# Performance work log

Measured on AMD Instinct MI355X. Metric: run time of the kernel, lower is better.

## Reference

```python
import jax, jax.numpy as jnp
import numpy as np

B, T, C, H = 8, 2048, 1024, 1024
SCALE = 1.0 / np.sqrt(H).astype(np.float32)


def setup_inputs() -> dict:
    key = jax.random.key(0)
    kx, kq, kk, kv = jax.random.split(key, 4)
    x = jax.random.normal(kx, (B, T, C), dtype=jnp.float32)
    # Linear(C -> H, bias=False): store weights as [C, H] so y = x @ W
    Wq = jax.random.normal(kq, (C, H), dtype=jnp.float32) * (1.0 / np.sqrt(C))
    Wk = jax.random.normal(kk, (C, H), dtype=jnp.float32) * (1.0 / np.sqrt(C))
    Wv = jax.random.normal(kv, (C, H), dtype=jnp.float32) * (1.0 / np.sqrt(C))
    return {"x": x, "Wq": Wq, "Wk": Wk, "Wv": Wv}


def reference(x, Wq, Wk, Wv):
    # Projections
    Q = jnp.einsum('btc,ch->bth', x, Wq)
    K = jnp.einsum('btc,ch->bth', x, Wk)
    V = jnp.einsum('btc,ch->bth', x, Wv)
    t = x.shape[1]
    # Scaled dot-product scores with causal mask
    attn = jnp.einsum('bqh,bkh->bqk', Q, K) * SCALE  # [B,T,T]
    causal = jnp.tril(jnp.ones((t, t), dtype=bool))
    attn = jnp.where(causal, attn, -jnp.inf)
    scores = jax.nn.softmax(attn, axis=-1)
    # dropout p=0.0 (eval/deterministic) -> identity
    out = jnp.einsum('bqk,bkh->bqh', scores, V)
    return out
```

## Files before the change

kernel.cpp:

```cpp
#include <hip/hip_runtime.h>


#define BM 128
#define BN 128
#define BK 32

typedef __attribute__((ext_vector_type(8))) __bf16 bf16x8;
typedef __attribute__((ext_vector_type(4))) float floatx4;

__device__ __forceinline__ unsigned short f2bf(float f) {
  unsigned int u = __float_as_uint(f);
  u += 0x7fffu + ((u >> 16) & 1u);
  return (unsigned short)(u >> 16);
}
__device__ __forceinline__ float bf2f(unsigned short s) {
  return __uint_as_float(((unsigned int)s) << 16);
}

__device__ __forceinline__ void gload_lds16(const unsigned short* g, unsigned short* l) {
  __builtin_amdgcn_global_load_lds(
      (const __attribute__((address_space(1))) void*)g,
      (__attribute__((address_space(3))) void*)l,
      16, 0, 0);
}


__device__ __forceinline__ void gemm_mainloop(
    const unsigned short* __restrict__ A, int lda,
    const unsigned short* __restrict__ Bt, int ldb,
    int m0, int n0, int kTiles,
    unsigned short* As, unsigned short* Bs,
    floatx4 (&acc)[4][4])
{
  const int tid  = threadIdx.x;
  const int wave = tid >> 6;
  const int lane = tid & 63;
  const int wr = wave >> 1;
  const int wc = wave & 1;

  const int c0 = wave * 2;
  const int c1 = c0 + 1;
  const int r0 = c0 * 16 + (lane >> 2);
  const int r1 = c1 * 16 + (lane >> 2);
  const int ck = (lane & 3) * 8;

  const unsigned short* pA0 = A  + (size_t)(m0 + r0) * lda + ck;
  const unsigned short* pA1 = A  + (size_t)(m0 + r1) * lda + ck;
  const unsigned short* pB0 = Bt + (size_t)(n0 + r0) * ldb + ck;
  const unsigned short* pB1 = Bt + (size_t)(n0 + r1) * ldb + ck;

  unsigned short* lA0 = As + c0 * 512;
  unsigned short* lA1 = As + c1 * 512;
  unsigned short* lB0 = Bs + c0 * 512;
  unsigned short* lB1 = Bs + c1 * 512;

  const int fr = lane & 15;
  const int kq = (lane >> 4) * 8;

  for (int kt = 0; kt < kTiles; ++kt) {
    __syncthreads();
    gload_lds16(pA0, lA0);
    gload_lds16(pA1, lA1);
    gload_lds16(pB0, lB0);
    gload_lds16(pB1, lB1);
    pA0 += BK; pA1 += BK; pB0 += BK; pB1 += BK;
    __syncthreads();

    bf16x8 af[4], bg[4];
#pragma unroll
    for (int i = 0; i < 4; ++i)
      af[i] = *(const bf16x8*)(As + ((wr * 64 + i * 16 + fr) * BK + kq));
#pragma unroll
    for (int j = 0; j < 4; ++j)
      bg[j] = *(const bf16x8*)(Bs + ((wc * 64 + j * 16 + fr) * BK + kq));
#pragma unroll
    for (int i = 0; i < 4; ++i)
#pragma unroll
      for (int j = 0; j < 4; ++j)
        acc[i][j] = __builtin_amdgcn_mfma_f32_16x16x32_bf16(af[i], bg[j], acc[i][j], 0, 0, 0);
  }
}

#define ACC_INIT(acc)                         \
  do {                                        \
    floatx4 z_ = {0.f, 0.f, 0.f, 0.f};        \
    _Pragma("unroll")                         \
    for (int i_ = 0; i_ < 4; ++i_)            \
      _Pragma("unroll")                       \
      for (int j_ = 0; j_ < 4; ++j_)          \
        acc[i_][j_] = z_;                     \
  } while (0)


__global__ void cvt_x_kernel(const float* __restrict__ x, unsigned short* __restrict__ xb) {
  int idx = (blockIdx.x * 256 + threadIdx.x) * 4;
  float4 v = *(const float4*)(x + idx);
  ushort4 o;
  o.x = f2bf(v.x); o.y = f2bf(v.y); o.z = f2bf(v.z); o.w = f2bf(v.w);
  *(ushort4*)(xb + idx) = o;
}

__global__ void cvt_w_kernel(const float* __restrict__ W, unsigned short* __restrict__ Wt) {
  __shared__ unsigned short tile[64][65];
  const int k0 = blockIdx.x * 64, n0 = blockIdx.y * 64;
  const int tid = threadIdx.x, tx = tid & 63, ty = tid >> 6;
#pragma unroll
  for (int r = 0; r < 64; r += 4)
    tile[r + ty][tx] = f2bf(W[(size_t)(k0 + r + ty) * 1024 + (n0 + tx)]);
  __syncthreads();
#pragma unroll
  for (int r = 0; r < 64; r += 4)
    Wt[(size_t)(n0 + r + ty) * 1024 + (k0 + tx)] = tile[tx][r + ty];
}

__global__ void zero_l_kernel(float* __restrict__ l) {
  l[blockIdx.x * 256 + threadIdx.x] = 0.f;
}

__global__ __launch_bounds__(512, 2) void gemm_qkv_kernel(
    const unsigned short* __restrict__ xb,
    const unsigned short* __restrict__ Wt,
    unsigned short* __restrict__ Q,
    unsigned short* __restrict__ K,
    unsigned short* __restrict__ V)
{
  __shared__ __align__(16) unsigned short lds[49152];

  const int bid = blockIdx.x;
  const int xcd = bid & 7;
  const int local = bid >> 3;
  const int mi = xcd * 8 + (local & 7);
  const int ni = local >> 3;
  const int m0 = mi * 256;
  const int n0 = ni * 256;

  const int tid = threadIdx.x;
  const int w = tid >> 6;
  const int l = tid & 63;
  const int wr = w >> 2;
  const int wc = w & 3;

  const int sr0 = w * 16 + (l >> 2);
  const int scs = (((l & 3) ^ ((l >> 3) & 3)) << 3);

  const unsigned short* pA0 = xb + (size_t)(m0 + sr0) * 1024 + scs;
  const unsigned short* pA1 = xb + (size_t)(m0 + 128 + sr0) * 1024 + scs;
  const unsigned short* pB0 = Wt + (size_t)(n0 + sr0) * 1024 + scs;
  const unsigned short* pB1 = Wt + (size_t)(n0 + 128 + sr0) * 1024 + scs;

  const int stgW = w * 512;

#define STAGE4(slot)                                             \
  do {                                                           \
    unsigned short* _sA = &lds[(slot) * 8192 + stgW];            \
    unsigned short* _sB = &lds[24576 + (slot) * 8192 + stgW];    \
    gload_lds16(pA0, _sA);                                       \
    gload_lds16(pA1, _sA + 4096);                                \
    gload_lds16(pB0, _sB);                                       \
    gload_lds16(pB1, _sB + 4096);                                \
    pA0 += 32; pA1 += 32; pB0 += 32; pB1 += 32;                  \
  } while (0)

  const int fr = l & 15;
  const int q  = l >> 4;
  const int cks = ((q ^ ((fr >> 1) & 3)) << 3);
  const int aOff = (wr * 128 + fr) * 32 + cks;
  const int bOff = (wc * 64 + fr) * 32 + cks;

  floatx4 acc[8][4];
  {
    floatx4 z = {0.f, 0.f, 0.f, 0.f};
#pragma unroll
    for (int i = 0; i < 8; ++i)
#pragma unroll
      for (int j = 0; j < 4; ++j)
        acc[i][j] = z;
  }

  STAGE4(0);
  STAGE4(1);
  asm volatile("s_waitcnt vmcnt(4)" ::: "memory");
  __builtin_amdgcn_s_barrier();

  bf16x8 a[8], b0[4], b1[4];
  {
    const unsigned short* sA = &lds[0];
    const unsigned short* sB = &lds[24576];
#pragma unroll
    for (int j = 0; j < 4; ++j) b0[j] = *(const bf16x8*)(sB + bOff + j * 512);
    a[0] = *(const bf16x8*)(sA + aOff);
    a[1] = *(const bf16x8*)(sA + aOff + 512);
  }

#define MFMA_PAIR(I0, BU)                                                           \
  do {                                                                              \
    __builtin_amdgcn_s_setprio(1);                                                  \
    _Pragma("unroll")                                                               \
    for (int j = 0; j < 4; ++j) {                                                   \
      acc[(I0)][j] =                                                                \
          __builtin_amdgcn_mfma_f32_16x16x32_bf16(a[(I0)], BU[j], acc[(I0)][j], 0, 0, 0); \
      acc[(I0) + 1][j] =                                                            \
          __builtin_amdgcn_mfma_f32_16x16x32_bf16(a[(I0) + 1], BU[j], acc[(I0) + 1][j], 0, 0, 0); \
    }                                                                               \
    __builtin_amdgcn_s_setprio(0);                                                  \
  } while (0)

#define ITER(KT, BU, BP)                                                  \
  do {                                                                    \
    const int nslot = (slot == 2) ? 0 : slot + 1;                         \
    const int sslot = (nslot == 2) ? 0 : nslot + 1;                       \
    const unsigned short* sA  = &lds[slot * 8192];                        \
    const unsigned short* sAn = &lds[nslot * 8192];                       \
    const unsigned short* sBn = &lds[24576 + nslot * 8192];               \
    unsigned short* dA = &lds[sslot * 8192 + stgW];                       \
    unsigned short* dB = &lds[24576 + sslot * 8192 + stgW];               \
    const bool doStage = ((KT) < 30);                                     \
    const bool doNext  = ((KT) < 31);                                     \
     \
    a[2] = *(const bf16x8*)(sA + aOff + 2 * 512);                         \
    a[3] = *(const bf16x8*)(sA + aOff + 3 * 512);                         \
    if (doStage) gload_lds16(pA0, dA);                                    \
    __builtin_amdgcn_s_barrier();                                         \
    MFMA_PAIR(0, BU);                                                     \
    __builtin_amdgcn_s_barrier();                                         \
                \
    a[4] = *(const bf16x8*)(sA + aOff + 4 * 512);                         \
    a[5] = *(const bf16x8*)(sA + aOff + 5 * 512);                         \
    if (doStage) gload_lds16(pA1, dA + 4096);                             \
    __builtin_amdgcn_s_barrier();                                         \
    MFMA_PAIR(2, BU);                                                     \
    __builtin_amdgcn_s_barrier();                                         \
                \
    a[6] = *(const bf16x8*)(sA + aOff + 6 * 512);                         \
    a[7] = *(const bf16x8*)(sA + aOff + 7 * 512);                         \
    if (doStage) gload_lds16(pB0, dB);                                    \
    __builtin_amdgcn_s_barrier();                                         \
    MFMA_PAIR(4, BU);                                                     \
    __builtin_amdgcn_s_barrier();                                         \
    \
    if (doNext) {                                                         \
      if (doStage) asm volatile("s_waitcnt vmcnt(3)" ::: "memory");       \
      else         asm volatile("s_waitcnt vmcnt(0)" ::: "memory");       \
      __builtin_amdgcn_s_barrier();                                       \
      _Pragma("unroll")                                                   \
      for (int j = 0; j < 4; ++j)                                         \
        BP[j] = *(const bf16x8*)(sBn + bOff + j * 512);                   \
      a[0] = *(const bf16x8*)(sAn + aOff);                                \
      a[1] = *(const bf16x8*)(sAn + aOff + 512);                          \
    }                                                                     \
    if (doStage) {                                                        \
      gload_lds16(pB1, dB + 4096);                                       \
      pA0 += 32; pA1 += 32; pB0 += 32; pB1 += 32;                         \
    }                                                                     \
    MFMA_PAIR(6, BU);                                                     \
    __builtin_amdgcn_s_barrier();                                         \
    slot = nslot;                                                         \
  } while (0)

  int slot = 0;
#pragma unroll 1
  for (int kt2 = 0; kt2 < 16; ++kt2) {
    const int kt = kt2 * 2;
    ITER(kt, b0, b1);
    ITER(kt + 1, b1, b0);
  }
#undef ITER
#undef MFMA_PAIR
#undef STAGE4

  unsigned short* const dsts[3] = {Q, K, V};
  unsigned short* D = dsts[n0 >> 10];
  const int ncol0 = n0 & 1023;

  const int rb = m0 + wr * 128 + (q << 2);
  const int cb = ncol0 + wc * 64 + fr;
#pragma unroll
  for (int i = 0; i < 8; ++i)
#pragma unroll
    for (int j = 0; j < 4; ++j)
#pragma unroll
      for (int r = 0; r < 4; ++r)
        D[(size_t)(rb + i * 16 + r) * 1024 + (cb + j * 16)] = f2bf(acc[i][j][r]);
}

__global__ void transpose_v_kernel(const unsigned short* __restrict__ V,
                                   unsigned short* __restrict__ Vt) {
  __shared__ unsigned short tile[64][68];
  const int b = blockIdx.z;
  const int t0 = blockIdx.x * 64, h0 = blockIdx.y * 64;
  const int tid = threadIdx.x;
  const int cx = (tid & 15) * 4;
  const int ry = tid >> 4;
  const unsigned short* Vb = V + (size_t)b * 2048 * 1024;
#pragma unroll
  for (int r = 0; r < 64; r += 16) {
    ushort4 v = *(const ushort4*)(Vb + (size_t)(t0 + r + ry) * 1024 + (h0 + cx));
    *(ushort4*)&tile[r + ry][cx] = v;
  }
  __syncthreads();
  unsigned short* Vtb = Vt + (size_t)b * 1024 * 2048;
#pragma unroll
  for (int r = 0; r < 64; r += 16) {
    const int h = r + ry;
    ushort4 o;
    o.x = tile[cx][h]; o.y = tile[cx + 1][h]; o.z = tile[cx + 2][h]; o.w = tile[cx + 3][h];
    *(ushort4*)(Vtb + (size_t)(h0 + h) * 2048 + (t0 + cx)) = o;
  }
}

__global__ __launch_bounds__(256) void gemm_scores_kernel(
    const unsigned short* __restrict__ Q,
    const unsigned short* __restrict__ K,
    unsigned short* __restrict__ S,
    float* __restrict__ lsum)
{
  const int b = blockIdx.x & 7;
  const int t = blockIdx.x >> 3;
  int mi = (int)((sqrtf(8.f * (float)t + 1.f) - 1.f) * 0.5f);
  while ((mi + 1) * (mi + 2) / 2 <= t) ++mi;
  while (mi * (mi + 1) / 2 > t) --mi;
  const int ni = t - mi * (mi + 1) / 2;
  const int m0 = mi * BM;
  const int n0 = ni * BN;

  __shared__ __align__(16) unsigned short As[BM * BK];
  __shared__ __align__(16) unsigned short Bs[BN * BK];
  floatx4 acc[4][4];
  ACC_INIT(acc);
  const unsigned short* Qb = Q + (size_t)b * 2048 * 1024;
  const unsigned short* Kb = K + (size_t)b * 2048 * 1024;
  gemm_mainloop(Qb, 1024, Kb, 1024, m0, n0, 1024 / BK, As, Bs, acc);

  unsigned short* Sb = S + (size_t)b * 2048 * 2048;
  float* lb = lsum + b * 2048;
  const int tid = threadIdx.x, wave = tid >> 6, lane = tid & 63;
  const int wr = wave >> 1, wc = wave & 1;
  const int rb = m0 + wr * 64 + ((lane >> 4) << 2);
  const int cb = n0 + wc * 64 + (lane & 15);

  float rsum[4][4];
#pragma unroll
  for (int i = 0; i < 4; ++i)
#pragma unroll
    for (int r = 0; r < 4; ++r)
      rsum[i][r] = 0.f;

#pragma unroll
  for (int i = 0; i < 4; ++i)
#pragma unroll
    for (int j = 0; j < 4; ++j)
#pragma unroll
      for (int r = 0; r < 4; ++r) {
        const int tq = rb + i * 16 + r;
        const int tk = cb + j * 16;
        float e = 0.f;
        if (tk <= tq) e = __expf(acc[i][j][r] * 0.03125f);
        const unsigned short h = f2bf(e);
        Sb[(size_t)tq * 2048 + tk] = h;
        rsum[i][r] += bf2f(h);
      }

#pragma unroll
  for (int off = 1; off < 16; off <<= 1)
#pragma unroll
    for (int i = 0; i < 4; ++i)
#pragma unroll
      for (int r = 0; r < 4; ++r)
        rsum[i][r] += __shfl_xor(rsum[i][r], off, 64);

  if ((lane & 15) == 0) {
#pragma unroll
    for (int i = 0; i < 4; ++i)
#pragma unroll
      for (int r = 0; r < 4; ++r)
        atomicAdd(&lb[rb + i * 16 + r], rsum[i][r]);
  }
}

__global__ __launch_bounds__(256) void gemm_pv_kernel(
    const unsigned short* __restrict__ S,
    const unsigned short* __restrict__ Vt,
    const float* __restrict__ lsum,
    float* __restrict__ out)
{
  const int b = blockIdx.x & 7;
  const int r2 = blockIdx.x >> 3;
  const int mi = 15 - (r2 >> 3);
  const int ni = r2 & 7;
  const int m0 = mi * BM;
  const int n0 = ni * BN;

  __shared__ __align__(16) unsigned short As[BM * BK];
  __shared__ __align__(16) unsigned short Bs[BN * BK];
  floatx4 acc[4][4];
  ACC_INIT(acc);
  const unsigned short* Pb = S  + (size_t)b * 2048 * 2048;
  const unsigned short* Vb = Vt + (size_t)b * 1024 * 2048;
  const int kTiles = m0 / BK + BM / BK;
  gemm_mainloop(Pb, 2048, Vb, 2048, m0, n0, kTiles, As, Bs, acc);

  float* Ob = out + (size_t)b * 2048 * 1024;
  const float* lb = lsum + b * 2048;
  const int tid = threadIdx.x, wave = tid >> 6, lane = tid & 63;
  const int wr = wave >> 1, wc = wave & 1;
  const int rb = m0 + wr * 64 + ((lane >> 4) << 2);
  const int cb = n0 + wc * 64 + (lane & 15);

  float inv[4][4];
#pragma unroll
  for (int i = 0; i < 4; ++i)
#pragma unroll
    for (int r = 0; r < 4; ++r)
      inv[i][r] = 1.0f / lb[rb + i * 16 + r];

#pragma unroll
  for (int i = 0; i < 4; ++i)
#pragma unroll
    for (int j = 0; j < 4; ++j)
#pragma unroll
      for (int r = 0; r < 4; ++r)
        Ob[(size_t)(rb + i * 16 + r) * 1024 + (cb + j * 16)] = acc[i][j][r] * inv[i][r];
}


extern "C" void kernel_launch(void* const* d_in, const int* in_sizes, int n_in,
                              void* d_out, int out_size, void* d_ws, size_t ws_size,
                              hipStream_t stream) {
  const float* x  = (const float*)d_in[0];
  const float* Wq = (const float*)d_in[1];
  const float* Wk = (const float*)d_in[2];
  const float* Wv = (const float*)d_in[3];
  float* out = (float*)d_out;

  char* ws = (char*)d_ws;
  unsigned short* xb  = (unsigned short*)(ws);
  unsigned short* Wt  = (unsigned short*)(ws + 33554432ull);
  unsigned short* Q   = (unsigned short*)(ws + 39845888ull);
  unsigned short* K   = (unsigned short*)(ws + 73400320ull);
  unsigned short* V   = (unsigned short*)(ws + 106954752ull);
  unsigned short* Vt  = (unsigned short*)(ws + 140509184ull);
  unsigned short* S   = (unsigned short*)(ws + 174063616ull);
  float*          l   = (float*)ws;

  cvt_x_kernel<<<16384, 256, 0, stream>>>(x, xb);
  dim3 gw(16, 16);
  cvt_w_kernel<<<gw, 256, 0, stream>>>(Wq, Wt);
  cvt_w_kernel<<<gw, 256, 0, stream>>>(Wk, Wt + 1024 * 1024);
  cvt_w_kernel<<<gw, 256, 0, stream>>>(Wv, Wt + 2 * 1024 * 1024);

  gemm_qkv_kernel<<<768, 512, 0, stream>>>(xb, Wt, Q, K, V);

  transpose_v_kernel<<<dim3(32, 16, 8), 256, 0, stream>>>(V, Vt);
  zero_l_kernel<<<64, 256, 0, stream>>>(l);
  gemm_scores_kernel<<<8 * 136, 256, 0, stream>>>(Q, K, S, l);
  gemm_pv_kernel<<<1024, 256, 0, stream>>>(S, Vt, l, out);
}
```

Baseline: 378.7 us.

## Widen attention GEMM K-tile to 64 with XOR-swizzled LDS and fuse prep kernels

The shared mainloop used by the scores and PV GEMMs now stages 64-wide K tiles instead of 32, using an XOR-swizzled LDS layout to avoid bank conflicts. This halves the number of barrier pairs per K step. The three conversion kernels and the zeroing kernel are merged into a single prep launch, and the row-sum buffer moves to its own workspace region instead of aliasing xb. The QKV macro's final staging load is moved into a helper macro and issued before the wait instead of after it, which changes the vmcnt accounting.

```diff
diff --git a/kernel.cpp b/kernel.cpp
--- a/kernel.cpp
+++ b/kernel.cpp
@@ -1,9 +1,5 @@
 #include <hip/hip_runtime.h>
 
-
-#define BM 128
-#define BN 128
-#define BK 32
 
 typedef __attribute__((ext_vector_type(8))) __bf16 bf16x8;
 typedef __attribute__((ext_vector_type(4))) float floatx4;
@@ -24,11 +20,10 @@
       16, 0, 0);
 }
 
-
-__device__ __forceinline__ void gemm_mainloop(
+__device__ __forceinline__ void gemm_mainloop64(
     const unsigned short* __restrict__ A, int lda,
     const unsigned short* __restrict__ Bt, int ldb,
-    int m0, int n0, int kTiles,
+    int m0, int n0, int kSteps,
     unsigned short* As, unsigned short* Bs,
     floatx4 (&acc)[4][4])
 {
@@ -38,41 +33,48 @@
   const int wr = wave >> 1;
   const int wc = wave & 1;
 
-  const int c0 = wave * 2;
-  const int c1 = c0 + 1;
-  const int r0 = c0 * 16 + (lane >> 2);
-  const int r1 = c1 * 16 + (lane >> 2);
-  const int ck = (lane & 3) * 8;
-
-  const unsigned short* pA0 = A  + (size_t)(m0 + r0) * lda + ck;
-  const unsigned short* pA1 = A  + (size_t)(m0 + r1) * lda + ck;
-  const unsigned short* pB0 = Bt + (size_t)(n0 + r0) * ldb + ck;
-  const unsigned short* pB1 = Bt + (size_t)(n0 + r1) * ldb + ck;
-
-  unsigned short* lA0 = As + c0 * 512;
-  unsigned short* lA1 = As + c1 * 512;
-  unsigned short* lB0 = Bs + c0 * 512;
-  unsigned short* lB1 = Bs + c1 * 512;
+  const int rowIn = lane >> 3;
+  const int srcChunk = (((lane & 7) ^ rowIn) << 3);
+
+  const unsigned short* gA = A  + (size_t)(m0 + wave * 32 + rowIn) * lda + srcChunk;
+  const unsigned short* gB = Bt + (size_t)(n0 + wave * 32 + rowIn) * ldb + srcChunk;
+  const int lda8 = lda << 3;
+  const int ldb8 = ldb << 3;
 
   const int fr = lane & 15;
-  const int kq = (lane >> 4) * 8;
-
-  for (int kt = 0; kt < kTiles; ++kt) {
+  const int kq = lane >> 4;
+  const int ac0 = ((kq ^ (fr & 7)) << 3);
+  const int ac1 = (((4 + kq) ^ (fr & 7)) << 3);
+
+  for (int kt = 0; kt < kSteps; ++kt) {
     __syncthreads();
-    gload_lds16(pA0, lA0);
-    gload_lds16(pA1, lA1);
-    gload_lds16(pB0, lB0);
-    gload_lds16(pB1, lB1);
-    pA0 += BK; pA1 += BK; pB0 += BK; pB1 += BK;
+#pragma unroll
+    for (int i = 0; i < 4; ++i)
+      gload_lds16(gA + i * lda8, As + (wave * 32 + i * 8) * 64);
+#pragma unroll
+    for (int i = 0; i < 4; ++i)
+      gload_lds16(gB + i * ldb8, Bs + (wave * 32 + i * 8) * 64);
+    gA += 64; gB += 64;
     __syncthreads();
 
     bf16x8 af[4], bg[4];
 #pragma unroll
     for (int i = 0; i < 4; ++i)
-      af[i] = *(const bf16x8*)(As + ((wr * 64 + i * 16 + fr) * BK + kq));
+      af[i] = *(const bf16x8*)(As + (wr * 64 + i * 16 + fr) * 64 + ac0);
 #pragma unroll
     for (int j = 0; j < 4; ++j)
-      bg[j] = *(const bf16x8*)(Bs + ((wc * 64 + j * 16 + fr) * BK + kq));
+      bg[j] = *(const bf16x8*)(Bs + (wc * 64 + j * 16 + fr) * 64 + ac0);
+#pragma unroll
+    for (int i = 0; i < 4; ++i)
+#pragma unroll
+      for (int j = 0; j < 4; ++j)
+        acc[i][j] = __builtin_amdgcn_mfma_f32_16x16x32_bf16(af[i], bg[j], acc[i][j], 0, 0, 0);
+#pragma unroll
+    for (int i = 0; i < 4; ++i)
+      af[i] = *(const bf16x8*)(As + (wr * 64 + i * 16 + fr) * 64 + ac1);
+#pragma unroll
+    for (int j = 0; j < 4; ++j)
+      bg[j] = *(const bf16x8*)(Bs + (wc * 64 + j * 16 + fr) * 64 + ac1);
 #pragma unroll
     for (int i = 0; i < 4; ++i)
 #pragma unroll
@@ -92,29 +94,41 @@
   } while (0)
 
 
-__global__ void cvt_x_kernel(const float* __restrict__ x, unsigned short* __restrict__ xb) {
-  int idx = (blockIdx.x * 256 + threadIdx.x) * 4;
-  float4 v = *(const float4*)(x + idx);
-  ushort4 o;
-  o.x = f2bf(v.x); o.y = f2bf(v.y); o.z = f2bf(v.z); o.w = f2bf(v.w);
-  *(ushort4*)(xb + idx) = o;
-}
-
-__global__ void cvt_w_kernel(const float* __restrict__ W, unsigned short* __restrict__ Wt) {
-  __shared__ unsigned short tile[64][65];
-  const int k0 = blockIdx.x * 64, n0 = blockIdx.y * 64;
-  const int tid = threadIdx.x, tx = tid & 63, ty = tid >> 6;
-#pragma unroll
-  for (int r = 0; r < 64; r += 4)
-    tile[r + ty][tx] = f2bf(W[(size_t)(k0 + r + ty) * 1024 + (n0 + tx)]);
-  __syncthreads();
-#pragma unroll
-  for (int r = 0; r < 64; r += 4)
-    Wt[(size_t)(n0 + r + ty) * 1024 + (k0 + tx)] = tile[tx][r + ty];
-}
-
-__global__ void zero_l_kernel(float* __restrict__ l) {
-  l[blockIdx.x * 256 + threadIdx.x] = 0.f;
+__global__ __launch_bounds__(256) void prep_kernel(
+    const float* __restrict__ x,
+    const float* __restrict__ Wq,
+    const float* __restrict__ Wk,
+    const float* __restrict__ Wv,
+    unsigned short* __restrict__ xb,
+    unsigned short* __restrict__ Wt,
+    float* __restrict__ l)
+{
+  const int bid = blockIdx.x;
+  const int tid = threadIdx.x;
+  if (bid < 16384) {
+    int idx = (bid * 256 + tid) * 4;
+    float4 v = *(const float4*)(x + idx);
+    ushort4 o;
+    o.x = f2bf(v.x); o.y = f2bf(v.y); o.z = f2bf(v.z); o.w = f2bf(v.w);
+    *(ushort4*)(xb + idx) = o;
+  } else if (bid < 17152) {
+    __shared__ unsigned short tile[64][65];
+    const int wb = bid - 16384;
+    const float* W = (wb < 256) ? Wq : (wb < 512) ? Wk : Wv;
+    unsigned short* Wtp = Wt + (size_t)(wb >> 8) * 1048576;
+    const int rem = wb & 255;
+    const int k0 = (rem & 15) * 64, n0 = (rem >> 4) * 64;
+    const int tx = tid & 63, ty = tid >> 6;
+#pragma unroll
+    for (int r = 0; r < 64; r += 4)
+      tile[r + ty][tx] = f2bf(W[(size_t)(k0 + r + ty) * 1024 + (n0 + tx)]);
+    __syncthreads();
+#pragma unroll
+    for (int r = 0; r < 64; r += 4)
+      Wtp[(size_t)(n0 + r + ty) * 1024 + (k0 + tx)] = tile[tx][r + ty];
+  } else {
+    l[(bid - 17152) * 256 + tid] = 0.f;
+  }
 }
 
 __global__ __launch_bounds__(512, 2) void gemm_qkv_kernel(
@@ -216,28 +230,25 @@
     unsigned short* dB = &lds[24576 + sslot * 8192 + stgW];               \
     const bool doStage = ((KT) < 30);                                     \
     const bool doNext  = ((KT) < 31);                                     \
-     \
     a[2] = *(const bf16x8*)(sA + aOff + 2 * 512);                         \
     a[3] = *(const bf16x8*)(sA + aOff + 3 * 512);                         \
     if (doStage) gload_lds16(pA0, dA);                                    \
     __builtin_amdgcn_s_barrier();                                         \
     MFMA_PAIR(0, BU);                                                     \
     __builtin_amdgcn_s_barrier();                                         \
-                \
     a[4] = *(const bf16x8*)(sA + aOff + 4 * 512);                         \
     a[5] = *(const bf16x8*)(sA + aOff + 5 * 512);                         \
     if (doStage) gload_lds16(pA1, dA + 4096);                             \
     __builtin_amdgcn_s_barrier();                                         \
     MFMA_PAIR(2, BU);                                                     \
     __builtin_amdgcn_s_barrier();                                         \
-                \
     a[6] = *(const bf16x8*)(sA + aOff + 6 * 512);                         \
     a[7] = *(const bf16x8*)(sA + aOff + 7 * 512);                         \
     if (doStage) gload_lds16(pB0, dB);                                    \
     __builtin_amdgcn_s_barrier();                                         \
     MFMA_PAIR(4, BU);                                                     \
     __builtin_amdgcn_s_barrier();                                         \
-    \
+    if (doStage) STAGE_LAST(dB);                                          \
     if (doNext) {                                                         \
       if (doStage) asm volatile("s_waitcnt vmcnt(3)" ::: "memory");       \
       else         asm volatile("s_waitcnt vmcnt(0)" ::: "memory");       \
@@ -248,13 +259,15 @@
       a[0] = *(const bf16x8*)(sAn + aOff);                                \
       a[1] = *(const bf16x8*)(sAn + aOff + 512);                          \
     }                                                                     \
-    if (doStage) {                                                        \
-      gload_lds16(pB1, dB + 4096);                                       \
-      pA0 += 32; pA1 += 32; pB0 += 32; pB1 += 32;                         \
-    }                                                                     \
     MFMA_PAIR(6, BU);                                                     \
     __builtin_amdgcn_s_barrier();                                         \
     slot = nslot;                                                         \
+  } while (0)
+
+#define STAGE_LAST(dB)                                                    \
+  do {                                                                    \
+    gload_lds16(pB1, (dB) + 4096);                                        \
+    pA0 += 32; pA1 += 32; pB0 += 32; pB1 += 32;                           \
   } while (0)
 
   int slot = 0;
@@ -265,6 +278,7 @@
     ITER(kt + 1, b1, b0);
   }
 #undef ITER
+#undef STAGE_LAST
 #undef MFMA_PAIR
 #undef STAGE4
 
@@ -320,16 +334,16 @@
   while ((mi + 1) * (mi + 2) / 2 <= t) ++mi;
   while (mi * (mi + 1) / 2 > t) --mi;
   const int ni = t - mi * (mi + 1) / 2;
-  const int m0 = mi * BM;
-  const int n0 = ni * BN;
-
-  __shared__ __align__(16) unsigned short As[BM * BK];
-  __shared__ __align__(16) unsigned short Bs[BN * BK];
+  const int m0 = mi * 128;
+  const int n0 = ni * 128;
+
+  __shared__ __align__(16) unsigned short As[128 * 64];
+  __shared__ __align__(16) unsigned short Bs[128 * 64];
   floatx4 acc[4][4];
   ACC_INIT(acc);
   const unsigned short* Qb = Q + (size_t)b * 2048 * 1024;
   const unsigned short* Kb = K + (size_t)b * 2048 * 1024;
-  gemm_mainloop(Qb, 1024, Kb, 1024, m0, n0, 1024 / BK, As, Bs, acc);
+  gemm_mainloop64(Qb, 1024, Kb, 1024, m0, n0, 16, As, Bs, acc);
 
   unsigned short* Sb = S + (size_t)b * 2048 * 2048;
   float* lb = lsum + b * 2048;
@@ -387,17 +401,17 @@
   const int r2 = blockIdx.x >> 3;
   const int mi = 15 - (r2 >> 3);
   const int ni = r2 & 7;
-  const int m0 = mi * BM;
-  const int n0 = ni * BN;
-
-  __shared__ __align__(16) unsigned short As[BM * BK];
-  __shared__ __align__(16) unsigned short Bs[BN * BK];
+  const int m0 = mi * 128;
+  const int n0 = ni * 128;
+
+  __shared__ __align__(16) unsigned short As[128 * 64];
+  __shared__ __align__(16) unsigned short Bs[128 * 64];
   floatx4 acc[4][4];
   ACC_INIT(acc);
   const unsigned short* Pb = S  + (size_t)b * 2048 * 2048;
   const unsigned short* Vb = Vt + (size_t)b * 1024 * 2048;
-  const int kTiles = m0 / BK + BM / BK;
-  gemm_mainloop(Pb, 2048, Vb, 2048, m0, n0, kTiles, As, Bs, acc);
+  const int kSteps = m0 / 64 + 2;
+  gemm_mainloop64(Pb, 2048, Vb, 2048, m0, n0, kSteps, As, Bs, acc);
 
   float* Ob = out + (size_t)b * 2048 * 1024;
   const float* lb = lsum + b * 2048;
@@ -440,18 +454,13 @@
   unsigned short* V   = (unsigned short*)(ws + 106954752ull);
   unsigned short* Vt  = (unsigned short*)(ws + 140509184ull);
   unsigned short* S   = (unsigned short*)(ws + 174063616ull);
-  float*          l   = (float*)ws;
-
-  cvt_x_kernel<<<16384, 256, 0, stream>>>(x, xb);
-  dim3 gw(16, 16);
-  cvt_w_kernel<<<gw, 256, 0, stream>>>(Wq, Wt);
-  cvt_w_kernel<<<gw, 256, 0, stream>>>(Wk, Wt + 1024 * 1024);
-  cvt_w_kernel<<<gw, 256, 0, stream>>>(Wv, Wt + 2 * 1024 * 1024);
+  float*          l   = (float*)(ws + 241172480ull);
+
+  prep_kernel<<<17216, 256, 0, stream>>>(x, Wq, Wk, Wv, xb, Wt, l);
 
   gemm_qkv_kernel<<<768, 512, 0, stream>>>(xb, Wt, Q, K, V);
 
   transpose_v_kernel<<<dim3(32, 16, 8), 256, 0, stream>>>(V, Vt);
-  zero_l_kernel<<<64, 256, 0, stream>>>(l);
   gemm_scores_kernel<<<8 * 136, 256, 0, stream>>>(Q, K, S, l);
   gemm_pv_kernel<<<1024, 256, 0, stream>>>(S, Vt, l, out);
 }
```

Result: faster. 350.7 us (-7.4%).
